# Kernel tuning notes

Measured on AMD Instinct MI355X. Metric: run time of the kernel, lower is better.

## Reference

```python
import jax, jax.numpy as jnp
import numpy as np

HEADS = 8
EPS = 1e-5


def layernorm(x, g, b):
    mu = jnp.mean(x, axis=-1, keepdims=True)
    var = jnp.mean((x - mu) ** 2, axis=-1, keepdims=True)
    return (x - mu) * jax.lax.rsqrt(var + EPS) * g + b


def setup_inputs() -> dict:
    key = jax.random.key(0)
    ks = jax.random.split(key, 5)
    B, C, H, W = 8, 384, 32, 32
    d = C
    s = 0.02
    return {
        "x": jax.random.normal(ks[0], (B, C, H, W), jnp.float32),
        "ln1_g": jnp.ones((d,), jnp.float32),
        "ln1_b": jnp.zeros((d,), jnp.float32),
        "lna_g": jnp.ones((d,), jnp.float32),
        "lna_b": jnp.zeros((d,), jnp.float32),
        "w_qkv": jax.random.normal(ks[1], (d, 3 * d), jnp.float32) * s,
        "w_out": jax.random.normal(ks[2], (d, d), jnp.float32) * s,
        "ln2_g": jnp.ones((d,), jnp.float32),
        "ln2_b": jnp.zeros((d,), jnp.float32),
        "w1": jax.random.normal(ks[3], (d, 4 * d), jnp.float32) * s,
        "b1": jnp.zeros((4 * d,), jnp.float32),
        "w2": jax.random.normal(ks[4], (4 * d, d), jnp.float32) * s,
        "b2": jnp.zeros((d,), jnp.float32),
    }


def reference(x, ln1_g, ln1_b, lna_g, lna_b, w_qkv, w_out, ln2_g, ln2_b, w1, b1, w2, b2):
    B, C, H, W = x.shape
    d = C
    dh = d // HEADS
    scale = dh ** (-0.5)
    # flatten spatial -> tokens: [B, N, C]
    t = x.reshape(B, C, H * W).transpose(0, 2, 1)

    # --- attention branch (note: double pre-norm, as in original) ---
    a = layernorm(t, ln1_g, ln1_b)
    a = layernorm(a, lna_g, lna_b)
    qkv = a @ w_qkv  # [B, N, 3d]
    q, k, v = jnp.split(qkv, 3, axis=-1)
    q = q.reshape(B, -1, HEADS, dh).transpose(0, 2, 1, 3)  # b h n d
    k = k.reshape(B, -1, HEADS, dh).transpose(0, 2, 1, 3)
    v = v.reshape(B, -1, HEADS, dh).transpose(0, 2, 1, 3)
    dots = jnp.einsum("bhnd,bhmd->bhnm", q, k) * scale
    attn = jax.nn.softmax(dots, axis=-1)
    o = jnp.einsum("bhnm,bhmd->bhnd", attn, v)
    o = o.transpose(0, 2, 1, 3).reshape(B, -1, d)
    t = t + o @ w_out

    # --- MLP branch (exact GELU, as torch nn.GELU default) ---
    m = layernorm(t, ln2_g, ln2_b)
    m = jax.nn.gelu(m @ w1 + b1, approximate=False) @ w2 + b2
    t = t + m

    return t.transpose(0, 2, 1).reshape(B, C, H, W)
```

## Files before the change

kernel.cpp:

```cpp
#include <hip/hip_runtime.h>
#include <math.h>

#define NTOK 1024
#define DM   384
#define NHEAD 8
#define DH   48
#define BATCH 8
#define NROWS (BATCH * NTOK)
#define SC2   (0.14433756729740643f * 1.4426950408889634f)

typedef __attribute__((ext_vector_type(8))) _Float16 f16x8;
typedef __attribute__((ext_vector_type(2))) __fp16 fp16x2_raw;
typedef __attribute__((ext_vector_type(4))) float f32x4;

#define ASYNC16(gp, lp) __builtin_amdgcn_global_load_lds( \
    (const __attribute__((address_space(1))) void*)(gp),  \
    (__attribute__((address_space(3))) void*)(lp), 16, 0, 0)

#define EXP2R(x) __builtin_amdgcn_exp2f(x)
#define RCPR(x)  __builtin_amdgcn_rcpf(x)

__device__ __forceinline__ unsigned int pkh(float a, float b) {
    union { fp16x2_raw h; unsigned int u; } cv;
    cv.h = __builtin_amdgcn_cvt_pkrtz(a, b);
    return cv.u;
}

__device__ __forceinline__ float gelu_fast(float v) {
    const float u = v * (0.7978845608f + 0.0356774081f * v * v);
    const float e = EXP2R(fminf(u * 2.885390082f, 120.0f));
    return v * e * RCPR(e + 1.0f);
}

__global__ __launch_bounds__(256) void prep_kernel(const float* __restrict__ x,
                                                   const float* __restrict__ ln1_g,
                                                   const float* __restrict__ ln1_b,
                                                   const float* __restrict__ lna_g,
                                                   const float* __restrict__ lna_b,
                                                   float* __restrict__ t,
                                                   _Float16* __restrict__ a_h,
                                                   const float* __restrict__ wqkv,
                                                   _Float16* __restrict__ wqkvT) {
    __shared__ float Ts[32][389];
    const int bid = blockIdx.x;
    const int tid = threadIdx.x;

    if (bid >= 256) {
        float (*tile)[33] = (float(*)[33])&Ts[0][0];
        const int tt = bid - 256;
        const int nx = 36;
        const int n0 = (tt % nx) * 32, k0 = (tt / nx) * 32;
        const int tx = tid & 31, ty = tid >> 5;
        #pragma unroll
        for (int i = ty; i < 32; i += 8)
            tile[i][tx] = wqkv[(size_t)(k0 + i) * 1152 + n0 + tx];
        __syncthreads();
        #pragma unroll
        for (int i = ty; i < 32; i += 8)
            wqkvT[(size_t)(n0 + i) * 384 + k0 + tx] = (_Float16)tile[tx][i];
        return;
    }

    const int b = bid >> 5, n0 = (bid & 31) * 32;
    const int tx = tid & 31, ty8 = tid >> 5;
    const float* xb = x + (size_t)b * (DM * NTOK);
    #pragma unroll
    for (int c0 = 0; c0 < DM; c0 += 32) {
        #pragma unroll
        for (int i = ty8; i < 32; i += 8)
            Ts[tx][c0 + i] = xb[(size_t)(c0 + i) * NTOK + n0 + tx];
    }
    __syncthreads();

    const int g = tid >> 3, sub = tid & 7;
    const int c0 = sub * 48;
    float xv[48];
    #pragma unroll
    for (int k = 0; k < 12; ++k)
        *(float4*)&xv[k * 4] = *(const float4*)&Ts[g][c0 + k * 4];

    const size_t trow = (size_t)((b << 10) + n0 + g) * DM;
    float s = 0.0f, sq = 0.0f;
    #pragma unroll
    for (int k = 0; k < 12; ++k)
        *(float4*)&t[trow + c0 + k * 4] = *(const float4*)&xv[k * 4];
    #pragma unroll
    for (int j = 0; j < 48; ++j) { s += xv[j]; sq += xv[j] * xv[j]; }
    s += __shfl_xor(s, 1, 64); sq += __shfl_xor(sq, 1, 64);
    s += __shfl_xor(s, 2, 64); sq += __shfl_xor(sq, 2, 64);
    s += __shfl_xor(s, 4, 64); sq += __shfl_xor(sq, 4, 64);
    float mu = s * (1.0f / DM);
    float var = fmaxf(sq * (1.0f / DM) - mu * mu, 0.0f);
    float r1 = rsqrtf(var + 1e-5f);

    float s2 = 0.0f, q2 = 0.0f;
    #pragma unroll
    for (int k = 0; k < 12; ++k) {
        const float4 gk = *(const float4*)&ln1_g[c0 + k * 4];
        const float4 bk = *(const float4*)&ln1_b[c0 + k * 4];
        float y0 = (xv[k*4+0] - mu) * r1 * gk.x + bk.x;
        float y1 = (xv[k*4+1] - mu) * r1 * gk.y + bk.y;
        float y2 = (xv[k*4+2] - mu) * r1 * gk.z + bk.z;
        float y3 = (xv[k*4+3] - mu) * r1 * gk.w + bk.w;
        xv[k*4+0] = y0; xv[k*4+1] = y1; xv[k*4+2] = y2; xv[k*4+3] = y3;
        s2 += (y0 + y1) + (y2 + y3);
        q2 += (y0*y0 + y1*y1) + (y2*y2 + y3*y3);
    }
    s2 += __shfl_xor(s2, 1, 64); q2 += __shfl_xor(q2, 1, 64);
    s2 += __shfl_xor(s2, 2, 64); q2 += __shfl_xor(q2, 2, 64);
    s2 += __shfl_xor(s2, 4, 64); q2 += __shfl_xor(q2, 4, 64);
    mu = s2 * (1.0f / DM);
    var = fmaxf(q2 * (1.0f / DM) - mu * mu, 0.0f);
    const float r2 = rsqrtf(var + 1e-5f);

    unsigned int d[12];
    #pragma unroll
    for (int k = 0; k < 12; ++k) {
        const float4 gk = *(const float4*)&lna_g[c0 + k * 4];
        const float4 bk = *(const float4*)&lna_b[c0 + k * 4];
        const float y0 = (xv[k*4+0] - mu) * r2 * gk.x + bk.x;
        const float y1 = (xv[k*4+1] - mu) * r2 * gk.y + bk.y;
        const float y2 = (xv[k*4+2] - mu) * r2 * gk.z + bk.z;
        const float y3 = (xv[k*4+3] - mu) * r2 * gk.w + bk.w;
        d[k*2+0] = pkh(y0, y1); d[k*2+1] = pkh(y2, y3);
    }
    unsigned int* op = (unsigned int*)(a_h + trow + c0);
    #pragma unroll
    for (int k = 0; k < 3; ++k)
        *(uint4*)(op + k * 4) = *(const uint4*)&d[k * 4];
}

template <int EPI>
__global__ __launch_bounds__(512, 4) void gemm8_f16(const _Float16* __restrict__ A,
                                                    const _Float16* __restrict__ Bt,
                                                    const float* __restrict__ bias,
                                                    _Float16* __restrict__ Ch,
                                                    int M, int N, int K) {
    __shared__ _Float16 As[2][128][64];
    __shared__ _Float16 Bs[2][192][64];
    const int tid = threadIdx.x;
    const int w = tid >> 6, lane = tid & 63;
    const int l15 = lane & 15, lq = lane >> 4;
    const int bm = blockIdx.y * 128, bn = blockIdx.x * 192;
    const int moff = (w & 1) * 64, noff = (w >> 1) * 48;

    const int srw = lane >> 3, pp = lane & 7;
    const int c = pp ^ srw;
    const _Float16* Ag[2];
    const _Float16* Bg[3];
    #pragma unroll
    for (int j = 0; j < 2; ++j)
        Ag[j] = A + (size_t)(bm + w * 16 + j * 8 + srw) * K + c * 8;
    #pragma unroll
    for (int j = 0; j < 3; ++j)
        Bg[j] = Bt + (size_t)(bn + w * 24 + j * 8 + srw) * K + c * 8;

    const int octA = ((lq ^ (l15 & 7)) << 4);

    f32x4 acc[4][3];
    #pragma unroll
    for (int mi = 0; mi < 4; ++mi)
        #pragma unroll
        for (int ni = 0; ni < 3; ++ni) acc[mi][ni] = (f32x4){0.f, 0.f, 0.f, 0.f};

    #pragma unroll
    for (int j = 0; j < 2; ++j) { ASYNC16(Ag[j], &As[0][w * 16 + j * 8][0]); Ag[j] += 64; }
    #pragma unroll
    for (int j = 0; j < 3; ++j) { ASYNC16(Bg[j], &Bs[0][w * 24 + j * 8][0]); Bg[j] += 64; }

    const int nkt = K >> 6;
    for (int kt = 0; kt < nkt; ++kt) {
        const int cur = kt & 1;
        __builtin_amdgcn_s_barrier();
        __builtin_amdgcn_sched_barrier(0);
        if (kt < nkt - 1) {
            #pragma unroll
            for (int j = 0; j < 2; ++j) { ASYNC16(Ag[j], &As[cur ^ 1][w * 16 + j * 8][0]); Ag[j] += 64; }
            #pragma unroll
            for (int j = 0; j < 3; ++j) { ASYNC16(Bg[j], &Bs[cur ^ 1][w * 24 + j * 8][0]); Bg[j] += 64; }
            asm volatile("s_waitcnt vmcnt(5)" ::: "memory");
        } else {
            asm volatile("s_waitcnt vmcnt(0)" ::: "memory");
        }
        __builtin_amdgcn_s_barrier();
        __builtin_amdgcn_sched_barrier(0);
        const char* Ab = (const char*)&As[cur][0][0];
        const char* Bb = (const char*)&Bs[cur][0][0];
        #pragma unroll
        for (int ks = 0; ks < 2; ++ks) {
            const int ox = octA ^ (ks << 6);
            f16x8 af[4], bfr[3];
            #pragma unroll
            for (int mi = 0; mi < 4; ++mi)
                af[mi] = *(const f16x8*)(Ab + ((moff + mi * 16 + l15) << 7) + ox);
            #pragma unroll
            for (int ni = 0; ni < 3; ++ni)
                bfr[ni] = *(const f16x8*)(Bb + ((noff + ni * 16 + l15) << 7) + ox);
            #pragma unroll
            for (int mi = 0; mi < 4; ++mi)
                #pragma unroll
                for (int ni = 0; ni < 3; ++ni)
                    acc[mi][ni] = __builtin_amdgcn_mfma_f32_16x16x32_f16(af[mi], bfr[ni], acc[mi][ni], 0, 0, 0);
        }
    }

    #pragma unroll
    for (int mi = 0; mi < 4; ++mi) {
        #pragma unroll
        for (int ni = 0; ni < 3; ++ni) {
            const int col = bn + noff + ni * 16 + l15;
            float bv = 0.0f;
            if (EPI == 2) bv = bias[col];
            #pragma unroll
            for (int r = 0; r < 4; ++r) {
                const int row = bm + moff + mi * 16 + lq * 4 + r;
                float v = acc[mi][ni][r];
                if (EPI == 2) v = gelu_fast(v + bv);
                Ch[(size_t)row * N + col] = (_Float16)v;
            }
        }
    }
}

template <int EPI, int BN>
__global__ __launch_bounds__(256, 2) void gemm_f16(const _Float16* __restrict__ A,
                                                   const _Float16* __restrict__ Bt,
                                                   const float* __restrict__ bias,
                                                   const float* __restrict__ R,
                                                   _Float16* __restrict__ Ch,
                                                   float* __restrict__ Cf,
                                                   int M, int N, int K) {
    constexpr int NFRAG = BN / 32;
    constexpr int NL = 4 + NFRAG;
    __shared__ _Float16 As[2][128][64];
    __shared__ _Float16 Bs[2][BN][64];
    const int tid = threadIdx.x;
    const int w = tid >> 6, lane = tid & 63;
    const int l15 = lane & 15, lq = lane >> 4;
    const int bm = blockIdx.y * 128, bn = blockIdx.x * BN;
    const int moff = (w & 1) * 64, noff = (w >> 1) * (BN / 2);

    const int srw = lane >> 3, pp = lane & 7;
    const int c = pp ^ srw;
    const _Float16* Ag[4];
    const _Float16* Bg[NFRAG];
    #pragma unroll
    for (int j = 0; j < 4; ++j)
        Ag[j] = A + (size_t)(bm + w * 32 + j * 8 + srw) * K + c * 8;
    #pragma unroll
    for (int j = 0; j < NFRAG; ++j)
        Bg[j] = Bt + (size_t)(bn + w * (BN / 4) + j * 8 + srw) * K + c * 8;

    const int octA = ((lq ^ (l15 & 7)) << 4);

    f32x4 acc[4][NFRAG];
    #pragma unroll
    for (int mi = 0; mi < 4; ++mi)
        #pragma unroll
        for (int ni = 0; ni < NFRAG; ++ni) acc[mi][ni] = (f32x4){0.f, 0.f, 0.f, 0.f};

    #pragma unroll
    for (int j = 0; j < 4; ++j) { ASYNC16(Ag[j], &As[0][w * 32 + j * 8][0]); Ag[j] += 64; }
    #pragma unroll
    for (int j = 0; j < NFRAG; ++j) { ASYNC16(Bg[j], &Bs[0][w * (BN / 4) + j * 8][0]); Bg[j] += 64; }

    const int nkt = K >> 6;
    for (int kt = 0; kt < nkt; ++kt) {
        const int cur = kt & 1;
        __builtin_amdgcn_s_barrier();
        __builtin_amdgcn_sched_barrier(0);
        if (kt < nkt - 1) {
            #pragma unroll
            for (int j = 0; j < 4; ++j) { ASYNC16(Ag[j], &As[cur ^ 1][w * 32 + j * 8][0]); Ag[j] += 64; }
            #pragma unroll
            for (int j = 0; j < NFRAG; ++j) { ASYNC16(Bg[j], &Bs[cur ^ 1][w * (BN / 4) + j * 8][0]); Bg[j] += 64; }
            asm volatile("s_waitcnt vmcnt(%0)" :: "n"(NL) : "memory");
        } else {
            asm volatile("s_waitcnt vmcnt(0)" ::: "memory");
        }
        __builtin_amdgcn_s_barrier();
        __builtin_amdgcn_sched_barrier(0);
        const char* Ab = (const char*)&As[cur][0][0];
        const char* Bb = (const char*)&Bs[cur][0][0];
        #pragma unroll
        for (int ks = 0; ks < 2; ++ks) {
            const int ox = octA ^ (ks << 6);
            f16x8 af[4], bfr[NFRAG];
            #pragma unroll
            for (int mi = 0; mi < 4; ++mi)
                af[mi] = *(const f16x8*)(Ab + ((moff + mi * 16 + l15) << 7) + ox);
            #pragma unroll
            for (int ni = 0; ni < NFRAG; ++ni)
                bfr[ni] = *(const f16x8*)(Bb + ((noff + ni * 16 + l15) << 7) + ox);
            #pragma unroll
            for (int mi = 0; mi < 4; ++mi)
                #pragma unroll
                for (int ni = 0; ni < NFRAG; ++ni)
                    acc[mi][ni] = __builtin_amdgcn_mfma_f32_16x16x32_f16(af[mi], bfr[ni], acc[mi][ni], 0, 0, 0);
        }
    }

    #pragma unroll
    for (int mi = 0; mi < 4; ++mi) {
        #pragma unroll
        for (int ni = 0; ni < NFRAG; ++ni) {
            const int col = bn + noff + ni * 16 + l15;
            float bv = 0.0f;
            if (EPI >= 2) bv = bias[col];
            if (EPI == 4) {
                const int row0 = bm + moff + mi * 16 + lq * 4;
                const int b = row0 >> 10, nn = row0 & 1023;
                float4 vv;
                vv.x = acc[mi][ni][0] + bv + R[(size_t)(row0 + 0) * N + col];
                vv.y = acc[mi][ni][1] + bv + R[(size_t)(row0 + 1) * N + col];
                vv.z = acc[mi][ni][2] + bv + R[(size_t)(row0 + 2) * N + col];
                vv.w = acc[mi][ni][3] + bv + R[(size_t)(row0 + 3) * N + col];
                *(float4*)(Cf + (size_t)b * (DM * NTOK) + (size_t)col * NTOK + nn) = vv;
            } else {
                #pragma unroll
                for (int r = 0; r < 4; ++r) {
                    const int row = bm + moff + mi * 16 + lq * 4 + r;
                    const size_t idx = (size_t)row * N + col;
                    float v = acc[mi][ni][r];
                    if (EPI == 2) v = gelu_fast(v + bv);
                    Ch[idx] = (_Float16)v;
                }
            }
        }
    }
}

__global__ __launch_bounds__(512) void gemm_out_ln(const _Float16* __restrict__ A,
                                                   const _Float16* __restrict__ Bt,
                                                   float* __restrict__ T,
                                                   _Float16* __restrict__ a_out,
                                                   const float* __restrict__ gg,
                                                   const float* __restrict__ bb) {
    __shared__ _Float16 As[2][32][64];
    __shared__ _Float16 Bs[2][384][64];
    __shared__ float red_s[8][16];
    __shared__ float red_q[8][16];
    const int tid = threadIdx.x;
    const int w = tid >> 6, lane = tid & 63;
    const int l15 = lane & 15, lq = lane >> 4;
    const int bm = blockIdx.x * 32;
    const int mr = (w & 1) * 16;
    const int cq = (w >> 1) * 96;

    const int srw = lane >> 3, pp = lane & 7;
    const int c = pp ^ srw;
    const _Float16* Ag = A + (size_t)(bm + w * 8 + srw) * 384 + c * 8;
    const _Float16* Bg[6];
    #pragma unroll
    for (int j = 0; j < 6; ++j)
        Bg[j] = Bt + (size_t)(j * 64 + w * 8 + srw) * 384 + c * 8;

    const int octA = ((lq ^ (l15 & 7)) << 4);

    f32x4 acc[6];
    #pragma unroll
    for (int ni = 0; ni < 6; ++ni) acc[ni] = (f32x4){0.f, 0.f, 0.f, 0.f};

    if (w < 4) { ASYNC16(Ag, &As[0][w * 8][0]); Ag += 64; }
    #pragma unroll
    for (int j = 0; j < 6; ++j) { ASYNC16(Bg[j], &Bs[0][j * 64 + w * 8][0]); Bg[j] += 64; }

    for (int kt = 0; kt < 6; ++kt) {
        const int cur = kt & 1;
        __builtin_amdgcn_s_barrier();
        __builtin_amdgcn_sched_barrier(0);
        if (kt < 5) {
            if (w < 4) { ASYNC16(Ag, &As[cur ^ 1][w * 8][0]); Ag += 64; }
            #pragma unroll
            for (int j = 0; j < 6; ++j) { ASYNC16(Bg[j], &Bs[cur ^ 1][j * 64 + w * 8][0]); Bg[j] += 64; }
            if (w < 4) asm volatile("s_waitcnt vmcnt(7)" ::: "memory");
            else       asm volatile("s_waitcnt vmcnt(6)" ::: "memory");
        } else {
            asm volatile("s_waitcnt vmcnt(0)" ::: "memory");
        }
        __builtin_amdgcn_s_barrier();
        __builtin_amdgcn_sched_barrier(0);
        #pragma unroll
        for (int ks = 0; ks < 2; ++ks) {
            const int ox = octA ^ (ks << 6);
            const f16x8 af = *(const f16x8*)((const char*)&As[cur][0][0] + ((mr + l15) << 7) + ox);
            #pragma unroll
            for (int ni = 0; ni < 6; ++ni) {
                const f16x8 bf = *(const f16x8*)((const char*)&Bs[cur][0][0] + ((cq + ni * 16 + l15) << 7) + ox);
                acc[ni] = __builtin_amdgcn_mfma_f32_16x16x32_f16(af, bf, acc[ni], 0, 0, 0);
            }
        }
    }

    float vv[6][4];
    float s[4] = {0.f, 0.f, 0.f, 0.f}, q[4] = {0.f, 0.f, 0.f, 0.f};
    #pragma unroll
    for (int ni = 0; ni < 6; ++ni) {
        const int col = cq + ni * 16 + l15;
        #pragma unroll
        for (int r = 0; r < 4; ++r) {
            const int row = bm + mr + lq * 4 + r;
            const float v = acc[ni][r] + T[(size_t)row * DM + col];
            vv[ni][r] = v;
            T[(size_t)row * DM + col] = v;
            s[r] += v; q[r] += v * v;
        }
    }
    #pragma unroll
    for (int off = 1; off < 16; off <<= 1) {
        #pragma unroll
        for (int r = 0; r < 4; ++r) {
            s[r] += __shfl_xor(s[r], off, 64);
            q[r] += __shfl_xor(q[r], off, 64);
        }
    }
    if (l15 == 0) {
        #pragma unroll
        for (int r = 0; r < 4; ++r) {
            red_s[w][lq * 4 + r] = s[r];
            red_q[w][lq * 4 + r] = q[r];
        }
    }
    __syncthreads();
    const int w0 = w & 1;
    float mu[4], rs[4];
    #pragma unroll
    for (int r = 0; r < 4; ++r) {
        const int i = lq * 4 + r;
        const float ts = (red_s[w0][i] + red_s[w0 + 2][i]) + (red_s[w0 + 4][i] + red_s[w0 + 6][i]);
        const float tq = (red_q[w0][i] + red_q[w0 + 2][i]) + (red_q[w0 + 4][i] + red_q[w0 + 6][i]);
        mu[r] = ts * (1.0f / DM);
        const float var = fmaxf(tq * (1.0f / DM) - mu[r] * mu[r], 0.0f);
        rs[r] = rsqrtf(var + 1e-5f);
    }
    #pragma unroll
    for (int ni = 0; ni < 6; ++ni) {
        const int col = cq + ni * 16 + l15;
        const float gv = gg[col], bv = bb[col];
        #pragma unroll
        for (int r = 0; r < 4; ++r) {
            const int row = bm + mr + lq * 4 + r;
            a_out[(size_t)row * DM + col] = (_Float16)((vv[ni][r] - mu[r]) * rs[r] * gv + bv);
        }
    }
}

__global__ __launch_bounds__(512, 4) void attn_kernel(const _Float16* __restrict__ qkv,
                                                      _Float16* __restrict__ o,
                                                      const float* __restrict__ wout,
                                                      const float* __restrict__ w1,
                                                      const float* __restrict__ w2,
                                                      _Float16* __restrict__ woutT,
                                                      _Float16* __restrict__ w1T,
                                                      _Float16* __restrict__ w2T) {
    __shared__ _Float16 Ks[2][64][64];
    __shared__ _Float16 Vt[2][48][72];
    __shared__ _Float16 Ps[8][16][72];
    const int tid = threadIdx.x;
    const int bid = blockIdx.x;

    if (bid >= 512) {
        const int half = tid >> 8;
        const int t8 = tid & 255;
        const int tx = t8 & 31, ty = t8 >> 5;
        const int idx = (bid - 512) * 2 + half;
        const float* W; _Float16* Wt; int K, N, nx, tt;
        if (idx < 144)      { W = wout; Wt = woutT; K = 384;  N = 384;  nx = 12; tt = idx; }
        else if (idx < 720) { W = w1;   Wt = w1T;   K = 384;  N = 1536; nx = 48; tt = idx - 144; }
        else                { W = w2;   Wt = w2T;   K = 1536; N = 384;  nx = 12; tt = idx - 720; }
        const int n0 = (tt % nx) * 32, k0 = (tt / nx) * 32;
        float (*tile)[33] = (float(*)[33])((char*)&Ks[0][0][0] + half * 4224);
        #pragma unroll
        for (int i = ty; i < 32; i += 8)
            tile[i][tx] = W[(size_t)(k0 + i) * N + n0 + tx];
        __syncthreads();
        #pragma unroll
        for (int i = ty; i < 32; i += 8)
            Wt[(size_t)(n0 + i) * K + k0 + tx] = (_Float16)tile[tx][i];
        return;
    }

    const int w = tid >> 6, lane = tid & 63;
    const int l15 = lane & 15, lq = lane >> 4;
    const int bh = ((bid >> 3) & 7) * 8 + (bid & 7);
    const int qt0 = (bid >> 6) * 128;
    const int h = bh & 7, b = bh >> 3;

    const _Float16* qbase = qkv + (size_t)b * NTOK * 1152 + h * 48;
    const _Float16* kbase = qbase + 384;
    const _Float16* vbase = qbase + 768;

    f16x8 qf[2];
    {
        const size_t qrow = (size_t)(qt0 + w * 16 + l15) * 1152;
        qf[0] = *(const f16x8*)(qbase + qrow + lq * 8);
        if (lq < 2) qf[1] = *(const f16x8*)(qbase + qrow + 32 + lq * 8);
        else        qf[1] = (f16x8){(_Float16)0, (_Float16)0, (_Float16)0, (_Float16)0,
                                    (_Float16)0, (_Float16)0, (_Float16)0, (_Float16)0};
    }

    const int srw = lane >> 3, pp = lane & 7;
    const int ck = pp ^ srw;
    const int ckoff = (ck < 6) ? ck * 8 : (ck - 6) * 8;
    const _Float16* Kg = kbase + (size_t)(w * 8 + srw) * 1152 + ckoff;
    const int vtp = tid & 31, vfo = tid >> 5;
    const _Float16* Vg = vbase + (size_t)(vtp * 2) * 1152 + vfo * 8;

    const int octK = ((lq ^ (l15 & 7)) << 4);

    ASYNC16(Kg, &Ks[0][w * 8][0]);
    Kg += 64 * 1152;
    uint4 va, vb;
    if (vfo < 6) { va = *(const uint4*)Vg; vb = *(const uint4*)(Vg + 1152); }
    Vg += 64 * 1152;

    f32x4 oacc[3];
    float lpart = 0.0f;
    #pragma unroll
    for (int vf = 0; vf < 3; ++vf) oacc[vf] = (f32x4){0.f, 0.f, 0.f, 0.f};

    int cur = 0;
    for (int kt = 0; kt < 16; ++kt) {
        if (vfo < 6) {
            const unsigned short* as = (const unsigned short*)&va;
            const unsigned short* bs = (const unsigned short*)&vb;
            #pragma unroll
            for (int j = 0; j < 8; ++j) {
                const unsigned int dw = (unsigned int)as[j] | ((unsigned int)bs[j] << 16);
                *(unsigned int*)((char*)&Vt[cur][0][0] + (vfo * 8 + j) * 144 + vtp * 4) = dw;
            }
        }
        __syncthreads();
        if (kt < 15) {
            ASYNC16(Kg, &Ks[cur ^ 1][w * 8][0]);
            Kg += 64 * 1152;
            if (vfo < 6) { va = *(const uint4*)Vg; vb = *(const uint4*)(Vg + 1152); }
            Vg += 64 * 1152;
        }

        f32x4 sacc[4];
        #pragma unroll
        for (int mi = 0; mi < 4; ++mi) sacc[mi] = (f32x4){0.f, 0.f, 0.f, 0.f};
        #pragma unroll
        for (int ks = 0; ks < 2; ++ks) {
            const int ox = octK ^ (ks << 6);
            #pragma unroll
            for (int mi = 0; mi < 4; ++mi) {
                const f16x8 kf = *(const f16x8*)((const char*)&Ks[cur][0][0] + ((mi * 16 + l15) << 7) + ox);
                sacc[mi] = __builtin_amdgcn_mfma_f32_16x16x32_f16(kf, qf[ks], sacc[mi], 0, 0, 0);
            }
        }

        #pragma unroll
        for (int mi = 0; mi < 4; ++mi) {
            const float p0 = EXP2R(sacc[mi][0] * SC2);
            const float p1 = EXP2R(sacc[mi][1] * SC2);
            const float p2 = EXP2R(sacc[mi][2] * SC2);
            const float p3 = EXP2R(sacc[mi][3] * SC2);
            lpart += (p0 + p1) + (p2 + p3);
            uint2 d;
            d.x = pkh(p0, p1); d.y = pkh(p2, p3);
            *(uint2*)((char*)&Ps[w][0][0] + l15 * 144 + (mi * 16 + lq * 4) * 2) = d;
        }
        asm volatile("s_waitcnt lgkmcnt(0)" ::: "memory");

        #pragma unroll
        for (int ks = 0; ks < 2; ++ks) {
            const int kk2 = ks * 64 + lq * 16;
            const f16x8 pf = *(const f16x8*)((const char*)&Ps[w][0][0] + l15 * 144 + kk2);
            #pragma unroll
            for (int vf = 0; vf < 3; ++vf) {
                const f16x8 vvv = *(const f16x8*)((const char*)&Vt[cur][0][0] + (vf * 16 + l15) * 144 + kk2);
                oacc[vf] = __builtin_amdgcn_mfma_f32_16x16x32_f16(vvv, pf, oacc[vf], 0, 0, 0);
            }
        }
        cur ^= 1;
    }

    lpart += __shfl_xor(lpart, 16, 64);
    lpart += __shfl_xor(lpart, 32, 64);
    const float linv = RCPR(lpart);
    _Float16* ob = o + (size_t)(b * NTOK + qt0 + w * 16 + l15) * DM + h * DH;
    #pragma unroll
    for (int vf = 0; vf < 3; ++vf) {
        uint2 d;
        d.x = pkh(oacc[vf][0] * linv, oacc[vf][1] * linv);
        d.y = pkh(oacc[vf][2] * linv, oacc[vf][3] * linv);
        *(uint2*)(ob + vf * 16 + lq * 4) = d;
    }
}

extern "C" void kernel_launch(void* const* d_in, const int* in_sizes, int n_in,
                              void* d_out, int out_size, void* d_ws, size_t ws_size,
                              hipStream_t stream) {
    const float* x     = (const float*)d_in[0];
    const float* ln1_g = (const float*)d_in[1];
    const float* ln1_b = (const float*)d_in[2];
    const float* lna_g = (const float*)d_in[3];
    const float* lna_b = (const float*)d_in[4];
    const float* w_qkv = (const float*)d_in[5];
    const float* w_out = (const float*)d_in[6];
    const float* ln2_g = (const float*)d_in[7];
    const float* ln2_b = (const float*)d_in[8];
    const float* w1    = (const float*)d_in[9];
    const float* b1    = (const float*)d_in[10];
    const float* w2    = (const float*)d_in[11];
    const float* b2    = (const float*)d_in[12];
    float* out = (float*)d_out;

    char* wsb = (char*)d_ws;
    float* t          = (float*)(wsb);
    _Float16* a_h     = (_Float16*)(wsb + 12582912);
    _Float16* qkv_h   = (_Float16*)(wsb + 18874368);
    _Float16* o_h     = (_Float16*)(wsb + 37748736);
    _Float16* h1_h    = (_Float16*)(wsb + 44040192);
    _Float16* wqkvT   = (_Float16*)(wsb + 69206016);
    _Float16* woutT   = (_Float16*)(wsb + 70090752);
    _Float16* w1T     = (_Float16*)(wsb + 70385664);
    _Float16* w2T     = (_Float16*)(wsb + 71565312);

    prep_kernel<<<256 + 432, 256, 0, stream>>>(x, ln1_g, ln1_b, lna_g, lna_b, t, a_h,
                                               w_qkv, wqkvT);
    gemm8_f16<0><<<dim3(6, 64), 512, 0, stream>>>(a_h, wqkvT, nullptr, qkv_h, NROWS, 3 * DM, DM);
    attn_kernel<<<512 + 648, 512, 0, stream>>>(qkv_h, o_h, w_out, w1, w2, woutT, w1T, w2T);
    gemm_out_ln<<<256, 512, 0, stream>>>(o_h, woutT, t, a_h, ln2_g, ln2_b);
    gemm8_f16<2><<<dim3(8, 64), 512, 0, stream>>>(a_h, w1T, b1, h1_h, NROWS, 4 * DM, DM);
    gemm_f16<4, 64><<<dim3(6, 64), 256, 0, stream>>>(h1_h, w2T, b2, t, nullptr, out, NROWS, DM, 4 * DM);
}
```

Before: 211.9 us.

## Retile final MLP down-projection GEMM to smaller 64x96 tiles with 8 waves

Replaces the 128x64-tile, 256-thread down-projection GEMM with a 64x96-tile, 512-thread kernel where each wave computes a 16x48 sub-tile. The grid grows from 384 to 512 blocks, aimed at better CU occupancy and fill across the GPU for this K=1536 GEMM. The trade-off is less operand reuse per wave (one A fragment shared by three B fragments) and more global/LDS traffic per FLOP.

```diff
diff --git a/kernel.cpp b/kernel.cpp
--- a/kernel.cpp
+++ b/kernel.cpp
@@ -222,47 +222,35 @@
     }
 }
 
-template <int EPI, int BN>
-__global__ __launch_bounds__(256, 2) void gemm_f16(const _Float16* __restrict__ A,
-                                                   const _Float16* __restrict__ Bt,
-                                                   const float* __restrict__ bias,
-                                                   const float* __restrict__ R,
-                                                   _Float16* __restrict__ Ch,
-                                                   float* __restrict__ Cf,
-                                                   int M, int N, int K) {
-    constexpr int NFRAG = BN / 32;
-    constexpr int NL = 4 + NFRAG;
-    __shared__ _Float16 As[2][128][64];
-    __shared__ _Float16 Bs[2][BN][64];
+__global__ __launch_bounds__(512, 4) void gemm8_mlp2(const _Float16* __restrict__ A,
+                                                     const _Float16* __restrict__ Bt,
+                                                     const float* __restrict__ bias,
+                                                     const float* __restrict__ R,
+                                                     float* __restrict__ Cf,
+                                                     int N, int K) {
+    __shared__ _Float16 As[2][64][64];
+    __shared__ _Float16 Bs[2][96][64];
     const int tid = threadIdx.x;
     const int w = tid >> 6, lane = tid & 63;
     const int l15 = lane & 15, lq = lane >> 4;
-    const int bm = blockIdx.y * 128, bn = blockIdx.x * BN;
-    const int moff = (w & 1) * 64, noff = (w >> 1) * (BN / 2);
+    const int wr = w & 3, wc = w >> 2;
+    const int bm = blockIdx.y * 64, bn = blockIdx.x * 96;
 
     const int srw = lane >> 3, pp = lane & 7;
     const int c = pp ^ srw;
-    const _Float16* Ag[4];
-    const _Float16* Bg[NFRAG];
-    #pragma unroll
-    for (int j = 0; j < 4; ++j)
-        Ag[j] = A + (size_t)(bm + w * 32 + j * 8 + srw) * K + c * 8;
-    #pragma unroll
-    for (int j = 0; j < NFRAG; ++j)
-        Bg[j] = Bt + (size_t)(bn + w * (BN / 4) + j * 8 + srw) * K + c * 8;
+    const _Float16* Ag  = A  + (size_t)(bm + w * 8 + srw) * K + c * 8;
+    const _Float16* Bg0 = Bt + (size_t)(bn + w * 8 + srw) * K + c * 8;
+    const _Float16* Bg1 = Bt + (size_t)(bn + 64 + w * 8 + srw) * K + c * 8;
 
     const int octA = ((lq ^ (l15 & 7)) << 4);
 
-    f32x4 acc[4][NFRAG];
-    #pragma unroll
-    for (int mi = 0; mi < 4; ++mi)
-        #pragma unroll
-        for (int ni = 0; ni < NFRAG; ++ni) acc[mi][ni] = (f32x4){0.f, 0.f, 0.f, 0.f};
-
-    #pragma unroll
-    for (int j = 0; j < 4; ++j) { ASYNC16(Ag[j], &As[0][w * 32 + j * 8][0]); Ag[j] += 64; }
-    #pragma unroll
-    for (int j = 0; j < NFRAG; ++j) { ASYNC16(Bg[j], &Bs[0][w * (BN / 4) + j * 8][0]); Bg[j] += 64; }
+    f32x4 acc[3];
+    #pragma unroll
+    for (int ni = 0; ni < 3; ++ni) acc[ni] = (f32x4){0.f, 0.f, 0.f, 0.f};
+
+    ASYNC16(Ag, &As[0][w * 8][0]); Ag += 64;
+    ASYNC16(Bg0, &Bs[0][w * 8][0]); Bg0 += 64;
+    if (w < 4) { ASYNC16(Bg1, &Bs[0][64 + w * 8][0]); Bg1 += 64; }
 
     const int nkt = K >> 6;
     for (int kt = 0; kt < nkt; ++kt) {
@@ -270,11 +258,14 @@
         __builtin_amdgcn_s_barrier();
         __builtin_amdgcn_sched_barrier(0);
         if (kt < nkt - 1) {
-            #pragma unroll
-            for (int j = 0; j < 4; ++j) { ASYNC16(Ag[j], &As[cur ^ 1][w * 32 + j * 8][0]); Ag[j] += 64; }
-            #pragma unroll
-            for (int j = 0; j < NFRAG; ++j) { ASYNC16(Bg[j], &Bs[cur ^ 1][w * (BN / 4) + j * 8][0]); Bg[j] += 64; }
-            asm volatile("s_waitcnt vmcnt(%0)" :: "n"(NL) : "memory");
+            ASYNC16(Ag, &As[cur ^ 1][w * 8][0]); Ag += 64;
+            ASYNC16(Bg0, &Bs[cur ^ 1][w * 8][0]); Bg0 += 64;
+            if (w < 4) {
+                ASYNC16(Bg1, &Bs[cur ^ 1][64 + w * 8][0]); Bg1 += 64;
+                asm volatile("s_waitcnt vmcnt(3)" ::: "memory");
+            } else {
+                asm volatile("s_waitcnt vmcnt(2)" ::: "memory");
+            }
         } else {
             asm volatile("s_waitcnt vmcnt(0)" ::: "memory");
         }
@@ -285,48 +276,27 @@
         #pragma unroll
         for (int ks = 0; ks < 2; ++ks) {
             const int ox = octA ^ (ks << 6);
-            f16x8 af[4], bfr[NFRAG];
-            #pragma unroll
-            for (int mi = 0; mi < 4; ++mi)
-                af[mi] = *(const f16x8*)(Ab + ((moff + mi * 16 + l15) << 7) + ox);
-            #pragma unroll
-            for (int ni = 0; ni < NFRAG; ++ni)
-                bfr[ni] = *(const f16x8*)(Bb + ((noff + ni * 16 + l15) << 7) + ox);
-            #pragma unroll
-            for (int mi = 0; mi < 4; ++mi)
-                #pragma unroll
-                for (int ni = 0; ni < NFRAG; ++ni)
-                    acc[mi][ni] = __builtin_amdgcn_mfma_f32_16x16x32_f16(af[mi], bfr[ni], acc[mi][ni], 0, 0, 0);
-        }
-    }
-
-    #pragma unroll
-    for (int mi = 0; mi < 4; ++mi) {
-        #pragma unroll
-        for (int ni = 0; ni < NFRAG; ++ni) {
-            const int col = bn + noff + ni * 16 + l15;
-            float bv = 0.0f;
-            if (EPI >= 2) bv = bias[col];
-            if (EPI == 4) {
-                const int row0 = bm + moff + mi * 16 + lq * 4;
-                const int b = row0 >> 10, nn = row0 & 1023;
-                float4 vv;
-                vv.x = acc[mi][ni][0] + bv + R[(size_t)(row0 + 0) * N + col];
-                vv.y = acc[mi][ni][1] + bv + R[(size_t)(row0 + 1) * N + col];
-                vv.z = acc[mi][ni][2] + bv + R[(size_t)(row0 + 2) * N + col];
-                vv.w = acc[mi][ni][3] + bv + R[(size_t)(row0 + 3) * N + col];
-                *(float4*)(Cf + (size_t)b * (DM * NTOK) + (size_t)col * NTOK + nn) = vv;
-            } else {
-                #pragma unroll
-                for (int r = 0; r < 4; ++r) {
-                    const int row = bm + moff + mi * 16 + lq * 4 + r;
-                    const size_t idx = (size_t)row * N + col;
-                    float v = acc[mi][ni][r];
-                    if (EPI == 2) v = gelu_fast(v + bv);
-                    Ch[idx] = (_Float16)v;
-                }
-            }
-        }
+            const f16x8 af = *(const f16x8*)(Ab + ((wr * 16 + l15) << 7) + ox);
+            #pragma unroll
+            for (int ni = 0; ni < 3; ++ni) {
+                const f16x8 bf = *(const f16x8*)(Bb + ((wc * 48 + ni * 16 + l15) << 7) + ox);
+                acc[ni] = __builtin_amdgcn_mfma_f32_16x16x32_f16(af, bf, acc[ni], 0, 0, 0);
+            }
+        }
+    }
+
+    #pragma unroll
+    for (int ni = 0; ni < 3; ++ni) {
+        const int col = bn + wc * 48 + ni * 16 + l15;
+        const float bv = bias[col];
+        const int row0 = bm + wr * 16 + lq * 4;
+        const int b = row0 >> 10, nn = row0 & 1023;
+        float4 vv;
+        vv.x = acc[ni][0] + bv + R[(size_t)(row0 + 0) * N + col];
+        vv.y = acc[ni][1] + bv + R[(size_t)(row0 + 1) * N + col];
+        vv.z = acc[ni][2] + bv + R[(size_t)(row0 + 2) * N + col];
+        vv.w = acc[ni][3] + bv + R[(size_t)(row0 + 3) * N + col];
+        *(float4*)(Cf + (size_t)b * (DM * NTOK) + (size_t)col * NTOK + nn) = vv;
     }
 }
 
@@ -625,5 +595,5 @@
     attn_kernel<<<512 + 648, 512, 0, stream>>>(qkv_h, o_h, w_out, w1, w2, woutT, w1T, w2T);
     gemm_out_ln<<<256, 512, 0, stream>>>(o_h, woutT, t, a_h, ln2_g, ln2_b);
     gemm8_f16<2><<<dim3(8, 64), 512, 0, stream>>>(a_h, w1T, b1, h1_h, NROWS, 4 * DM, DM);
-    gemm_f16<4, 64><<<dim3(6, 64), 256, 0, stream>>>(h1_h, w2T, b2, t, nullptr, out, NROWS, DM, 4 * DM);
-}
+    gemm8_mlp2<<<dim3(4, 128), 512, 0, stream>>>(h1_h, w2T, b2, t, out, DM, 4 * DM);
+}
```

Result: no change. 212.1 us (+0.1%).
